# Performance work log

Hardware: AMD Instinct MI355X
Metric: run time of the kernel (lower is better)

## Reference

```python
import jax, jax.numpy as jnp
import numpy as np

BT, N, C, H, W = 1, 4, 64, 28, 60
ZC, YC, XC = 200, 8, 200  # grid dims (Zcam, Ycam, Xcam); voxel_shape=[200,200,8] -> Z=200, X=200, Y=8
OUT_C = 128
EPS = 1e-6


def setup_inputs() -> dict:
    key = jax.random.key(0)
    k1, k2, k3, k4 = jax.random.split(key, 4)
    # normalized sampling coords in ~[-1.2, 1.2] so some points fall outside the image (zero-padded)
    voxcam_coords = jax.random.uniform(k1, (BT, N, ZC, YC, XC, 3), jnp.float32, -1.2, 1.2)
    # binary visibility mask per voxel-camera pair
    vox_valid = (jax.random.uniform(k2, (BT, N, ZC, YC, XC, 1)) < 0.5).astype(jnp.float32)
    img_feats = jax.random.normal(k3, (BT, N, C, H, W), jnp.float32)
    W_comp = jax.random.normal(k4, (OUT_C, C * YC), jnp.float32) * 0.02  # MLP-as-1x1-conv height compressor
    b_comp = jnp.zeros((OUT_C,), jnp.float32)
    return {"voxcam_coords": voxcam_coords, "vox_valid": vox_valid, "img_feats": img_feats,
            "W_comp": W_comp, "b_comp": b_comp}


def _grid_sample_3d(feat, grid):
    """Trilinear grid_sample, align_corners=False, zeros padding.
    feat: (B, C, D, H, W); grid: (B, P, 3) with (x, y, z) in [-1, 1]. Returns (B, C, P)."""
    B, Cc, D, Hh, Ww = feat.shape
    x = ((grid[..., 0] + 1.0) * Ww - 1.0) * 0.5
    y = ((grid[..., 1] + 1.0) * Hh - 1.0) * 0.5
    z = ((grid[..., 2] + 1.0) * D - 1.0) * 0.5
    x0f, y0f, z0f = jnp.floor(x), jnp.floor(y), jnp.floor(z)
    wx, wy, wz = x - x0f, y - y0f, z - z0f
    x0, y0, z0 = x0f.astype(jnp.int32), y0f.astype(jnp.int32), z0f.astype(jnp.int32)

    def sample_one(fb, x0b, y0b, z0b, wxb, wyb, wzb):
        out = jnp.zeros((Cc, x0b.shape[0]), fb.dtype)
        for dz in (0, 1):
            for dy in (0, 1):
                for dx in (0, 1):
                    zi, yi, xi = z0b + dz, y0b + dy, x0b + dx
                    valid = ((zi >= 0) & (zi < D) & (yi >= 0) & (yi < Hh)
                             & (xi >= 0) & (xi < Ww)).astype(fb.dtype)
                    v = fb[:, jnp.clip(zi, 0, D - 1), jnp.clip(yi, 0, Hh - 1), jnp.clip(xi, 0, Ww - 1)]
                    w = ((wxb if dx else 1.0 - wxb) * (wyb if dy else 1.0 - wyb)
                         * (wzb if dz else 1.0 - wzb)) * valid
                    out = out + v * w[None]
        return out

    return jax.vmap(sample_one)(feat, x0, y0, z0, wx, wy, wz)


def reference(voxcam_coords, vox_valid, img_feats, W_comp, b_comp):
    bt, n, zc, yc, xc, _ = voxcam_coords.shape
    c, h, w = img_feats.shape[2], img_feats.shape[3], img_feats.shape[4]
    P = zc * yc * xc
    grid = voxcam_coords.reshape(bt * n, P, 3)
    feat = img_feats.reshape(bt * n, c, 1, h, w)  # N_group=1 depth axis
    sampled = _grid_sample_3d(feat, grid).reshape(bt, n, c, zc, yc, xc)
    mask = jnp.transpose(vox_valid, (0, 1, 5, 2, 3, 4))  # (bt, n, 1, zc, yc, xc)
    vox_feats = sampled * mask                      # get_feats_dense_grid_sample masking
    # reduce_cams: masked mean over cameras (dim=1)
    red = (vox_feats * mask).sum(axis=1) / (mask.sum(axis=1) + EPS)  # (bt, c, zc, yc, xc)
    # height compressor: 'bt c z y x -> bt (c y) z x' then 1x1 conv (MLP)
    comp_in = jnp.transpose(red, (0, 1, 3, 2, 4)).reshape(bt, c * yc, zc, xc)
    out = jnp.einsum('bczx,oc->bozx', comp_in, W_comp) + b_comp[None, :, None, None]
    # _unpack_batch: (b*t, C, Z, X) -> (b, t, C, Z, X) with b=t=1
    return out.reshape(1, bt, out.shape[1], zc, xc)
```

## Files before the change

### kernel.cpp

```cpp
#include <hip/hip_runtime.h>
#include <hip/hip_bf16.h>
#include <hip/hip_fp16.h>

#define N_  4
#define C_  64
#define H_  28
#define W_  60
#define ZC_ 200
#define YC_ 8
#define XC_ 200
#define OUTC_ 128
#define KD_ 512
#define EPS_ 1e-6f
#define ZB 4
#define XB 8
#define NCOL 32

typedef __attribute__((ext_vector_type(8))) _Float16 half8;
typedef __attribute__((ext_vector_type(4))) float f32x4;
typedef __attribute__((ext_vector_type(4))) unsigned int u32x4;

__global__ void gsvt_prep(const float* __restrict__ img,
                          const float* __restrict__ Wc,
                          __half* __restrict__ featH,
                          __half* __restrict__ WbH) {
    int tid = blockIdx.x * blockDim.x + threadIdx.x;
    int stride = gridDim.x * blockDim.x;
    const int totF = N_ * H_ * W_ * C_;
    for (int i = tid; i < totF; i += stride) {
        int c  = i & 63;
        int hw = i >> 6;
        int w  = hw % W_;
        int nh = hw / W_;
        int h  = nh % H_;
        int n  = nh / H_;
        featH[i] = __float2half(img[((n * C_ + c) * H_ + h) * W_ + w]);
    }
    const int totW = OUTC_ * KD_;
    for (int i = tid; i < totW; i += stride) {
        int k = i & (KD_ - 1);
        int o = i >> 9;
        int y = k >> 6;
        int c = k & 63;
        WbH[i] = __float2half(Wc[o * KD_ + c * YC_ + y]);
    }
}

__device__ __forceinline__ void accq(__half2* n, const u32x4 V, const unsigned wp) {
    const __half2 w2 = *(const __half2*)&wp;
    unsigned vx = V.x, vy = V.y, vz = V.z, vw = V.w;
    n[0] = __hfma2(w2, *(const __half2*)&vx, n[0]);
    n[1] = __hfma2(w2, *(const __half2*)&vy, n[1]);
    n[2] = __hfma2(w2, *(const __half2*)&vz, n[2]);
    n[3] = __hfma2(w2, *(const __half2*)&vw, n[3]);
}

__device__ __forceinline__ unsigned reph(float f) {
    auto h = __builtin_amdgcn_cvt_pkrtz(f, f);
    unsigned u;
    __builtin_memcpy(&u, &h, 4);
    return u;
}

__global__ __launch_bounds__(256, 4) void gsvt_fusedG(
        const float* __restrict__ coords,
        const float* __restrict__ validm,
        const __half* __restrict__ featH,
        const __half* __restrict__ WbH,
        const float* __restrict__ bias,
        float* __restrict__ out)
{
    __shared__ uint2 tab2[N_ * 256];
    __shared__ unsigned short redB[64][NCOL][8];
    float (*ms)[4] = (float(*)[4])&redB[0][0][0];

    const int z0 = blockIdx.y * ZB;
    const int x0 = blockIdx.x * XB;
    const int t  = threadIdx.x;

    const int p0   = t;
    const int y0_  = t >> 5;
    const int col0 = t & 31;
    const int zg   = z0 + (col0 >> 3);
    const int xg   = x0 + (col0 & 7);

    float gx[4], gy[4], gzv[4], mm[4];
    #pragma unroll
    for (int cam = 0; cam < N_; ++cam) {
        const int cb = ((cam * ZC_ + zg) * YC_ + y0_) * XC_ + xg;
        gx[cam]  = coords[cb * 3 + 0];
        gy[cam]  = coords[cb * 3 + 1];
        gzv[cam] = coords[cb * 3 + 2];
        mm[cam]  = validm[cb];
        ms[p0][cam] = mm[cam];
    }
    __syncthreads();

    {
        const float inv = 1.0f / (ms[p0][0] + ms[p0][1] + ms[p0][2] + ms[p0][3] + EPS_);
        #pragma unroll
        for (int cam = 0; cam < N_; ++cam) {
            const float xf = ((gx[cam] + 1.0f) * (float)W_ - 1.0f) * 0.5f;
            const float yf = ((gy[cam] + 1.0f) * (float)H_ - 1.0f) * 0.5f;
            const float zf = gzv[cam] * 0.5f;
            const float x0f = floorf(xf), y0f = floorf(yf), z0f = floorf(zf);
            const float wx = xf - x0f, wy = yf - y0f, wz = zf - z0f;
            const int xi = (int)x0f, yi = (int)y0f, zi = (int)z0f;

            const float zw = (zi == 0) ? (1.f - wz) : ((zi == -1) ? wz : 0.f);
            const float s  = mm[cam] * zw * inv;

            const float wx0 = (xi >= 0 && xi < W_)         ? (1.f - wx) * s : 0.f;
            const float wx1 = (xi + 1 >= 0 && xi + 1 < W_) ? wx * s         : 0.f;
            const float wy0 = (yi >= 0 && yi < H_)         ? (1.f - wy)     : 0.f;
            const float wy1 = (yi + 1 >= 0 && yi + 1 < H_) ? wy             : 0.f;

            const unsigned q00 = (unsigned)(wy0 * wx0 * 4095.f + 0.5f);
            const unsigned q01 = (unsigned)(wy0 * wx1 * 4095.f + 0.5f);
            const unsigned q10 = (unsigned)(wy1 * wx0 * 4095.f + 0.5f);
            const unsigned q11 = (unsigned)(wy1 * wx1 * 4095.f + 0.5f);

            const int xc0 = min(max(xi, 0), W_ - 1);
            const int xc1 = min(max(xi + 1, 0), W_ - 1);
            const int yc0 = min(max(yi, 0), H_ - 1);
            const int yc1 = min(max(yi + 1, 0), H_ - 1);
            const unsigned pixidx = (unsigned)((cam * H_ + yc0) * W_ + xc0);
            const unsigned fdx = (unsigned)(xc1 - xc0);
            const unsigned fdy = (unsigned)(yc1 - yc0);

            const unsigned A = q00 | (q01 << 12) | ((q10 & 0xFFu) << 24);
            const unsigned B = (q10 >> 8) | (q11 << 4) | (pixidx << 16)
                             | (fdx << 29) | (fdy << 30);
            tab2[cam * 256 + p0] = make_uint2(A, B);
        }
    }
    __syncthreads();

    const int grp   = t >> 3;
    const int lane8 = t & 7;
    const unsigned lb = (unsigned)(lane8 << 4);
    const char* fb = (const char*)featH;

    #define ISSUE(V, A_) asm volatile("global_load_dwordx4 %0, %1, off" \
                                      : "=v"(V) : "v"(A_))
    #define WAITV(n) do { asm volatile("s_waitcnt vmcnt(" #n ")"); \
                          __builtin_amdgcn_sched_barrier(0); } while (0)

    #pragma unroll
    for (int y = 0; y < YC_; ++y) {
        const int p = y * 32 + grp;

        const uint2 T0 = tab2[0 * 256 + p];
        const uint2 T1 = tab2[1 * 256 + p];
        const uint2 T2 = tab2[2 * 256 + p];
        const uint2 T3 = tab2[3 * 256 + p];

        u32x4 V00, V01, V02, V03, V10, V11, V12, V13;
        u32x4 V20, V21, V22, V23, V30, V31, V32, V33;
        #define ADDR_ISSUE(Tv, Va, Vb, Vc, Vd)                                 \
            {                                                                  \
                const bool act = (Tv.x | (Tv.y & 0xFFFFu)) != 0u;              \
                const unsigned base = act ? ((((Tv.y >> 16) & 0x1FFFu) << 7) + lb) : lb; \
                const unsigned dxo  = act ? (((Tv.y >> 29) & 1u) << 7) : 0u;   \
                const unsigned dyo  = act ? (((Tv.y >> 30) & 1u) * (unsigned)(W_ * 128)) : 0u; \
                ISSUE(Va, fb + base);                                          \
                ISSUE(Vb, fb + (base + dxo));                                  \
                ISSUE(Vc, fb + (base + dyo));                                  \
                ISSUE(Vd, fb + (base + dyo + dxo));                            \
            }
        ADDR_ISSUE(T0, V00, V01, V02, V03)
        ADDR_ISSUE(T1, V10, V11, V12, V13)
        ADDR_ISSUE(T2, V20, V21, V22, V23)
        ADDR_ISSUE(T3, V30, V31, V32, V33)
        #undef ADDR_ISSUE

        __half2 zz2 = __half2half2(__ushort_as_half(0));
        __half2 num[4] = {zz2, zz2, zz2, zz2};

        #define DECW(Tv, w00, w01, w10, w11)                                   \
            const unsigned w00 = reph((float)(Tv.x & 0xFFFu)            * (1.f/4095.f)); \
            const unsigned w01 = reph((float)((Tv.x >> 12) & 0xFFFu)    * (1.f/4095.f)); \
            const unsigned w10 = reph((float)((Tv.x >> 24) | ((Tv.y & 0xFu) << 8)) * (1.f/4095.f)); \
            const unsigned w11 = reph((float)((Tv.y >> 4) & 0xFFFu)     * (1.f/4095.f));

        { DECW(T0, a, b, c, d) WAITV(12);
          accq(num, V00, a); accq(num, V01, b); accq(num, V02, c); accq(num, V03, d); }
        { DECW(T1, a, b, c, d) WAITV(8);
          accq(num, V10, a); accq(num, V11, b); accq(num, V12, c); accq(num, V13, d); }
        { DECW(T2, a, b, c, d) WAITV(4);
          accq(num, V20, a); accq(num, V21, b); accq(num, V22, c); accq(num, V23, d); }
        { DECW(T3, a, b, c, d) WAITV(0);
          accq(num, V30, a); accq(num, V31, b); accq(num, V32, c); accq(num, V33, d); }
        #undef DECW

        const int kb   = y * 8 + lane8;
        const int pcol = (grp & 16) | ((grp ^ kb) & 15);
        unsigned n0 = *(unsigned*)&num[0], n1 = *(unsigned*)&num[1];
        unsigned n2 = *(unsigned*)&num[2], n3 = *(unsigned*)&num[3];
        *(uint4*)&redB[kb][pcol][0] = make_uint4(n0, n1, n2, n3);
    }
    #undef ISSUE
    #undef WAITV
    __syncthreads();

    const int wave = t >> 6;
    const int lane = t & 63;
    const int q    = lane >> 4;
    const int l16  = lane & 15;

    f32x4 acc00 = {0.f,0.f,0.f,0.f}, acc01 = {0.f,0.f,0.f,0.f};
    f32x4 acc10 = {0.f,0.f,0.f,0.f}, acc11 = {0.f,0.f,0.f,0.f};
    const __half* wbase = WbH + (wave * 32 + l16) * KD_;

    #pragma unroll
    for (int ks = 0; ks < 16; ++ks) {
        const int kb = ks * 4 + q;
        const int xs = l16 ^ (kb & 15);
        const half8 Bf0 = *(const half8*)&redB[kb][xs][0];
        const half8 Bf1 = *(const half8*)&redB[kb][16 + xs][0];
        const half8 Af0 = *(const half8*)(wbase + ks * 32 + q * 8);
        const half8 Af1 = *(const half8*)(wbase + 16 * KD_ + ks * 32 + q * 8);
        acc00 = __builtin_amdgcn_mfma_f32_16x16x32_f16(Af0, Bf0, acc00, 0, 0, 0);
        acc01 = __builtin_amdgcn_mfma_f32_16x16x32_f16(Af0, Bf1, acc01, 0, 0, 0);
        acc10 = __builtin_amdgcn_mfma_f32_16x16x32_f16(Af1, Bf0, acc10, 0, 0, 0);
        acc11 = __builtin_amdgcn_mfma_f32_16x16x32_f16(Af1, Bf1, acc11, 0, 0, 0);
    }

    #pragma unroll
    for (int ct = 0; ct < 2; ++ct) {
        const int c2  = ct * 16 + l16;
        const int zz  = c2 >> 3;
        const int xl  = c2 & 7;
        const int ob  = (z0 + zz) * XC_ + x0 + xl;
        const f32x4 a0 = ct ? acc01 : acc00;
        const f32x4 a1 = ct ? acc11 : acc10;
        #pragma unroll
        for (int j = 0; j < 4; ++j) {
            const int o0 = wave * 32 + q * 4 + j;
            out[o0 * (ZC_ * XC_) + ob] = a0[j] + bias[o0];
            const int o1 = o0 + 16;
            out[o1 * (ZC_ * XC_) + ob] = a1[j] + bias[o1];
        }
    }
}

extern "C" void kernel_launch(void* const* d_in, const int* in_sizes, int n_in,
                              void* d_out, int out_size, void* d_ws, size_t ws_size,
                              hipStream_t stream) {
    const float* coords = (const float*)d_in[0];
    const float* validm = (const float*)d_in[1];
    const float* img    = (const float*)d_in[2];
    const float* Wc     = (const float*)d_in[3];
    const float* bias   = (const float*)d_in[4];
    float* out = (float*)d_out;

    __half* featH = (__half*)d_ws;
    __half* WbH   = featH + (N_ * H_ * W_ * C_);

    gsvt_prep<<<512, 256, 0, stream>>>(img, Wc, featH, WbH);

    dim3 grid(XC_ / XB, ZC_ / ZB);
    gsvt_fusedG<<<grid, 256, 0, stream>>>(coords, validm, featH, WbH, bias, out);
}
```

Before: 56.13 us.

## Split fused sample+GEMM kernel into separate sampling and MFMA GEMM kernels

Splits the fused kernel in two when the workspace is large enough. A gather kernel writes the reduced fp16 features to global memory, and a separate GEMM kernel keeps the weights in registers and runs MFMA over tiles of 16 points. This removes the large LDS reduction buffer from the gather kernel, which raises its occupancy target to 6 blocks, and lets the GEMM reuse its weights across tiles. The cost is a global round trip of about 41 MB of intermediate data plus one extra kernel launch.

```diff
diff --git a/kernel.cpp b/kernel.cpp
--- a/kernel.cpp
+++ b/kernel.cpp
@@ -15,6 +15,8 @@
 #define ZB 4
 #define XB 8
 #define NCOL 32
+#define NPTS 40000
+#define TPB_GEMM 4
 
 typedef __attribute__((ext_vector_type(8))) _Float16 half8;
 typedef __attribute__((ext_vector_type(4))) float f32x4;
@@ -62,6 +64,203 @@
     return u;
 }
 
+__device__ __forceinline__ void phase0_tab(const float* __restrict__ coords,
+                                           const float* __restrict__ validm,
+                                           uint2* tab2, float (*ms)[4],
+                                           int z0, int x0, int t) {
+    const int p0   = t;
+    const int y0_  = t >> 5;
+    const int col0 = t & 31;
+    const int zg   = z0 + (col0 >> 3);
+    const int xg   = x0 + (col0 & 7);
+
+    float gx[4], gy[4], gzv[4], mm[4];
+    #pragma unroll
+    for (int cam = 0; cam < N_; ++cam) {
+        const int cb = ((cam * ZC_ + zg) * YC_ + y0_) * XC_ + xg;
+        gx[cam]  = coords[cb * 3 + 0];
+        gy[cam]  = coords[cb * 3 + 1];
+        gzv[cam] = coords[cb * 3 + 2];
+        mm[cam]  = validm[cb];
+        ms[p0][cam] = mm[cam];
+    }
+    __syncthreads();
+
+    const float inv = 1.0f / (ms[p0][0] + ms[p0][1] + ms[p0][2] + ms[p0][3] + EPS_);
+    #pragma unroll
+    for (int cam = 0; cam < N_; ++cam) {
+        const float xf = ((gx[cam] + 1.0f) * (float)W_ - 1.0f) * 0.5f;
+        const float yf = ((gy[cam] + 1.0f) * (float)H_ - 1.0f) * 0.5f;
+        const float zf = gzv[cam] * 0.5f;
+        const float x0f = floorf(xf), y0f = floorf(yf), z0f = floorf(zf);
+        const float wx = xf - x0f, wy = yf - y0f, wz = zf - z0f;
+        const int xi = (int)x0f, yi = (int)y0f, zi = (int)z0f;
+
+        const float zw = (zi == 0) ? (1.f - wz) : ((zi == -1) ? wz : 0.f);
+        const float s  = mm[cam] * zw * inv;
+
+        const float wx0 = (xi >= 0 && xi < W_)         ? (1.f - wx) * s : 0.f;
+        const float wx1 = (xi + 1 >= 0 && xi + 1 < W_) ? wx * s         : 0.f;
+        const float wy0 = (yi >= 0 && yi < H_)         ? (1.f - wy)     : 0.f;
+        const float wy1 = (yi + 1 >= 0 && yi + 1 < H_) ? wy             : 0.f;
+
+        const unsigned q00 = (unsigned)(wy0 * wx0 * 4095.f + 0.5f);
+        const unsigned q01 = (unsigned)(wy0 * wx1 * 4095.f + 0.5f);
+        const unsigned q10 = (unsigned)(wy1 * wx0 * 4095.f + 0.5f);
+        const unsigned q11 = (unsigned)(wy1 * wx1 * 4095.f + 0.5f);
+
+        const int xc0 = min(max(xi, 0), W_ - 1);
+        const int xc1 = min(max(xi + 1, 0), W_ - 1);
+        const int yc0 = min(max(yi, 0), H_ - 1);
+        const int yc1 = min(max(yi + 1, 0), H_ - 1);
+        const unsigned pixidx = (unsigned)((cam * H_ + yc0) * W_ + xc0);
+        const unsigned fdx = (unsigned)(xc1 - xc0);
+        const unsigned fdy = (unsigned)(yc1 - yc0);
+
+        const unsigned A = q00 | (q01 << 12) | ((q10 & 0xFFu) << 24);
+        const unsigned B = (q10 >> 8) | (q11 << 4) | (pixidx << 16)
+                         | (fdx << 29) | (fdy << 30);
+        tab2[cam * 256 + p0] = make_uint2(A, B);
+    }
+    __syncthreads();
+}
+
+#define GATHER_BODY(P_, OUTSTMT)                                               \
+    {                                                                          \
+        const uint2 T0 = tab2[0 * 256 + (P_)];                                 \
+        const uint2 T1 = tab2[1 * 256 + (P_)];                                 \
+        const uint2 T2 = tab2[2 * 256 + (P_)];                                 \
+        const uint2 T3 = tab2[3 * 256 + (P_)];                                 \
+        u32x4 V00, V01, V02, V03, V10, V11, V12, V13;                          \
+        u32x4 V20, V21, V22, V23, V30, V31, V32, V33;                          \
+        ADDR_ISSUE(T0, V00, V01, V02, V03)                                     \
+        ADDR_ISSUE(T1, V10, V11, V12, V13)                                     \
+        ADDR_ISSUE(T2, V20, V21, V22, V23)                                     \
+        ADDR_ISSUE(T3, V30, V31, V32, V33)                                     \
+        __half2 zz2 = __half2half2(__ushort_as_half(0));                       \
+        __half2 num[4] = {zz2, zz2, zz2, zz2};                                 \
+        { DECW(T0, a, b, c, d) WAITV(12);                                      \
+          accq(num, V00, a); accq(num, V01, b);                                \
+          accq(num, V02, c); accq(num, V03, d); }                              \
+        { DECW(T1, a, b, c, d) WAITV(8);                                       \
+          accq(num, V10, a); accq(num, V11, b);                                \
+          accq(num, V12, c); accq(num, V13, d); }                              \
+        { DECW(T2, a, b, c, d) WAITV(4);                                       \
+          accq(num, V20, a); accq(num, V21, b);                                \
+          accq(num, V22, c); accq(num, V23, d); }                              \
+        { DECW(T3, a, b, c, d) WAITV(0);                                       \
+          accq(num, V30, a); accq(num, V31, b);                                \
+          accq(num, V32, c); accq(num, V33, d); }                              \
+        unsigned n0 = *(unsigned*)&num[0], n1 = *(unsigned*)&num[1];           \
+        unsigned n2 = *(unsigned*)&num[2], n3 = *(unsigned*)&num[3];           \
+        OUTSTMT;                                                               \
+    }
+
+#define ADDR_ISSUE(Tv, Va, Vb, Vc, Vd)                                         \
+    {                                                                          \
+        const bool act = (Tv.x | (Tv.y & 0xFFFFu)) != 0u;                      \
+        const unsigned base = act ? ((((Tv.y >> 16) & 0x1FFFu) << 7) + lb) : lb; \
+        const unsigned dxo  = act ? (((Tv.y >> 29) & 1u) << 7) : 0u;           \
+        const unsigned dyo  = act ? (((Tv.y >> 30) & 1u) * (unsigned)(W_ * 128)) : 0u; \
+        ISSUE(Va, fb + base);                                                  \
+        ISSUE(Vb, fb + (base + dxo));                                          \
+        ISSUE(Vc, fb + (base + dyo));                                          \
+        ISSUE(Vd, fb + (base + dyo + dxo));                                    \
+    }
+#define ISSUE(V, A_) asm volatile("global_load_dwordx4 %0, %1, off" \
+                                  : "=v"(V) : "v"(A_))
+#define WAITV(n) do { asm volatile("s_waitcnt vmcnt(" #n ")"); \
+                      __builtin_amdgcn_sched_barrier(0); } while (0)
+#define DECW(Tv, w00, w01, w10, w11)                                           \
+    const unsigned w00 = reph((float)(Tv.x & 0xFFFu)            * (1.f/4095.f)); \
+    const unsigned w01 = reph((float)((Tv.x >> 12) & 0xFFFu)    * (1.f/4095.f)); \
+    const unsigned w10 = reph((float)((Tv.x >> 24) | ((Tv.y & 0xFu) << 8)) * (1.f/4095.f)); \
+    const unsigned w11 = reph((float)((Tv.y >> 4) & 0xFFFu)     * (1.f/4095.f));
+
+__global__ __launch_bounds__(256, 6) void gsvt_sampleH(
+        const float* __restrict__ coords,
+        const float* __restrict__ validm,
+        const __half* __restrict__ featH,
+        __half* __restrict__ red)
+{
+    __shared__ uint2 tab2[N_ * 256];
+    __shared__ float ms[256][4];
+
+    const int z0 = blockIdx.y * ZB;
+    const int x0 = blockIdx.x * XB;
+    const int t  = threadIdx.x;
+
+    phase0_tab(coords, validm, tab2, ms, z0, x0, t);
+
+    const int grp   = t >> 3;
+    const int lane8 = t & 7;
+    const unsigned lb = (unsigned)(lane8 << 4);
+    const char* fb = (const char*)featH;
+    const int pt0 = (z0 + (grp >> 3)) * XC_ + x0 + (grp & 7);
+
+    #pragma unroll
+    for (int y = 0; y < YC_; ++y) {
+        const int p  = y * 32 + grp;
+        const int kb = y * 8 + lane8;
+        GATHER_BODY(p,
+            *(uint4*)(red + ((size_t)kb * NPTS + pt0) * 8) =
+                make_uint4(n0, n1, n2, n3))
+    }
+}
+
+__global__ __launch_bounds__(256, 2) void gsvt_gemmH(
+        const __half* __restrict__ red,
+        const __half* __restrict__ WbH,
+        const float* __restrict__ bias,
+        float* __restrict__ out)
+{
+    const int t    = threadIdx.x;
+    const int wave = t >> 6;
+    const int lane = t & 63;
+    const int q    = lane >> 4;
+    const int l16  = lane & 15;
+
+    half8 A0[16], A1[16];
+    const __half* wrow0 = WbH + (wave * 32 + l16) * KD_;
+    #pragma unroll
+    for (int ks = 0; ks < 16; ++ks) {
+        A0[ks] = *(const half8*)(wrow0 + ks * 32 + q * 8);
+        A1[ks] = *(const half8*)(wrow0 + 16 * KD_ + ks * 32 + q * 8);
+    }
+    float bs0[4], bs1[4];
+    #pragma unroll
+    for (int j = 0; j < 4; ++j) {
+        bs0[j] = bias[wave * 32 + q * 4 + j];
+        bs1[j] = bias[wave * 32 + q * 4 + j + 16];
+    }
+
+    for (int tt = 0; tt < TPB_GEMM; ++tt) {
+        const int n0 = (blockIdx.x * TPB_GEMM + tt) * 16;
+
+        half8 Bf[16];
+        #pragma unroll
+        for (int ks = 0; ks < 16; ++ks) {
+            const int kb = ks * 4 + q;
+            Bf[ks] = *(const half8*)(red + ((size_t)kb * NPTS + n0 + l16) * 8);
+        }
+
+        f32x4 acc0 = {0.f,0.f,0.f,0.f};
+        f32x4 acc1 = {0.f,0.f,0.f,0.f};
+        #pragma unroll
+        for (int ks = 0; ks < 16; ++ks) {
+            acc0 = __builtin_amdgcn_mfma_f32_16x16x32_f16(A0[ks], Bf[ks], acc0, 0, 0, 0);
+            acc1 = __builtin_amdgcn_mfma_f32_16x16x32_f16(A1[ks], Bf[ks], acc1, 0, 0, 0);
+        }
+
+        #pragma unroll
+        for (int j = 0; j < 4; ++j) {
+            const int o0 = wave * 32 + q * 4 + j;
+            out[(size_t)o0 * NPTS + n0 + l16] = acc0[j] + bs0[j];
+            out[(size_t)(o0 + 16) * NPTS + n0 + l16] = acc1[j] + bs1[j];
+        }
+    }
+}
+
 __global__ __launch_bounds__(256, 4) void gsvt_fusedG(
         const float* __restrict__ coords,
         const float* __restrict__ validm,
@@ -78,129 +277,21 @@
     const int x0 = blockIdx.x * XB;
     const int t  = threadIdx.x;
 
-    const int p0   = t;
-    const int y0_  = t >> 5;
-    const int col0 = t & 31;
-    const int zg   = z0 + (col0 >> 3);
-    const int xg   = x0 + (col0 & 7);
-
-    float gx[4], gy[4], gzv[4], mm[4];
-    #pragma unroll
-    for (int cam = 0; cam < N_; ++cam) {
-        const int cb = ((cam * ZC_ + zg) * YC_ + y0_) * XC_ + xg;
-        gx[cam]  = coords[cb * 3 + 0];
-        gy[cam]  = coords[cb * 3 + 1];
-        gzv[cam] = coords[cb * 3 + 2];
-        mm[cam]  = validm[cb];
-        ms[p0][cam] = mm[cam];
-    }
-    __syncthreads();
-
-    {
-        const float inv = 1.0f / (ms[p0][0] + ms[p0][1] + ms[p0][2] + ms[p0][3] + EPS_);
-        #pragma unroll
-        for (int cam = 0; cam < N_; ++cam) {
-            const float xf = ((gx[cam] + 1.0f) * (float)W_ - 1.0f) * 0.5f;
-            const float yf = ((gy[cam] + 1.0f) * (float)H_ - 1.0f) * 0.5f;
-            const float zf = gzv[cam] * 0.5f;
-            const float x0f = floorf(xf), y0f = floorf(yf), z0f = floorf(zf);
-            const float wx = xf - x0f, wy = yf - y0f, wz = zf - z0f;
-            const int xi = (int)x0f, yi = (int)y0f, zi = (int)z0f;
-
-            const float zw = (zi == 0) ? (1.f - wz) : ((zi == -1) ? wz : 0.f);
-            const float s  = mm[cam] * zw * inv;
-
-            const float wx0 = (xi >= 0 && xi < W_)         ? (1.f - wx) * s : 0.f;
-            const float wx1 = (xi + 1 >= 0 && xi + 1 < W_) ? wx * s         : 0.f;
-            const float wy0 = (yi >= 0 && yi < H_)         ? (1.f - wy)     : 0.f;
-            const float wy1 = (yi + 1 >= 0 && yi + 1 < H_) ? wy             : 0.f;
-
-            const unsigned q00 = (unsigned)(wy0 * wx0 * 4095.f + 0.5f);
-            const unsigned q01 = (unsigned)(wy0 * wx1 * 4095.f + 0.5f);
-            const unsigned q10 = (unsigned)(wy1 * wx0 * 4095.f + 0.5f);
-            const unsigned q11 = (unsigned)(wy1 * wx1 * 4095.f + 0.5f);
-
-            const int xc0 = min(max(xi, 0), W_ - 1);
-            const int xc1 = min(max(xi + 1, 0), W_ - 1);
-            const int yc0 = min(max(yi, 0), H_ - 1);
-            const int yc1 = min(max(yi + 1, 0), H_ - 1);
-            const unsigned pixidx = (unsigned)((cam * H_ + yc0) * W_ + xc0);
-            const unsigned fdx = (unsigned)(xc1 - xc0);
-            const unsigned fdy = (unsigned)(yc1 - yc0);
-
-            const unsigned A = q00 | (q01 << 12) | ((q10 & 0xFFu) << 24);
-            const unsigned B = (q10 >> 8) | (q11 << 4) | (pixidx << 16)
-                             | (fdx << 29) | (fdy << 30);
-            tab2[cam * 256 + p0] = make_uint2(A, B);
-        }
-    }
-    __syncthreads();
+    phase0_tab(coords, validm, tab2, ms, z0, x0, t);
 
     const int grp   = t >> 3;
     const int lane8 = t & 7;
     const unsigned lb = (unsigned)(lane8 << 4);
     const char* fb = (const char*)featH;
 
-    #define ISSUE(V, A_) asm volatile("global_load_dwordx4 %0, %1, off" \
-                                      : "=v"(V) : "v"(A_))
-    #define WAITV(n) do { asm volatile("s_waitcnt vmcnt(" #n ")"); \
-                          __builtin_amdgcn_sched_barrier(0); } while (0)
-
     #pragma unroll
     for (int y = 0; y < YC_; ++y) {
-        const int p = y * 32 + grp;
-
-        const uint2 T0 = tab2[0 * 256 + p];
-        const uint2 T1 = tab2[1 * 256 + p];
-        const uint2 T2 = tab2[2 * 256 + p];
-        const uint2 T3 = tab2[3 * 256 + p];
-
-        u32x4 V00, V01, V02, V03, V10, V11, V12, V13;
-        u32x4 V20, V21, V22, V23, V30, V31, V32, V33;
-        #define ADDR_ISSUE(Tv, Va, Vb, Vc, Vd)                                 \
-            {                                                                  \
-                const bool act = (Tv.x | (Tv.y & 0xFFFFu)) != 0u;              \
-                const unsigned base = act ? ((((Tv.y >> 16) & 0x1FFFu) << 7) + lb) : lb; \
-                const unsigned dxo  = act ? (((Tv.y >> 29) & 1u) << 7) : 0u;   \
-                const unsigned dyo  = act ? (((Tv.y >> 30) & 1u) * (unsigned)(W_ * 128)) : 0u; \
-                ISSUE(Va, fb + base);                                          \
-                ISSUE(Vb, fb + (base + dxo));                                  \
-                ISSUE(Vc, fb + (base + dyo));                                  \
-                ISSUE(Vd, fb + (base + dyo + dxo));                            \
-            }
-        ADDR_ISSUE(T0, V00, V01, V02, V03)
-        ADDR_ISSUE(T1, V10, V11, V12, V13)
-        ADDR_ISSUE(T2, V20, V21, V22, V23)
-        ADDR_ISSUE(T3, V30, V31, V32, V33)
-        #undef ADDR_ISSUE
-
-        __half2 zz2 = __half2half2(__ushort_as_half(0));
-        __half2 num[4] = {zz2, zz2, zz2, zz2};
-
-        #define DECW(Tv, w00, w01, w10, w11)                                   \
-            const unsigned w00 = reph((float)(Tv.x & 0xFFFu)            * (1.f/4095.f)); \
-            const unsigned w01 = reph((float)((Tv.x >> 12) & 0xFFFu)    * (1.f/4095.f)); \
-            const unsigned w10 = reph((float)((Tv.x >> 24) | ((Tv.y & 0xFu) << 8)) * (1.f/4095.f)); \
-            const unsigned w11 = reph((float)((Tv.y >> 4) & 0xFFFu)     * (1.f/4095.f));
-
-        { DECW(T0, a, b, c, d) WAITV(12);
-          accq(num, V00, a); accq(num, V01, b); accq(num, V02, c); accq(num, V03, d); }
-        { DECW(T1, a, b, c, d) WAITV(8);
-          accq(num, V10, a); accq(num, V11, b); accq(num, V12, c); accq(num, V13, d); }
-        { DECW(T2, a, b, c, d) WAITV(4);
-          accq(num, V20, a); accq(num, V21, b); accq(num, V22, c); accq(num, V23, d); }
-        { DECW(T3, a, b, c, d) WAITV(0);
-          accq(num, V30, a); accq(num, V31, b); accq(num, V32, c); accq(num, V33, d); }
-        #undef DECW
-
+        const int p    = y * 32 + grp;
         const int kb   = y * 8 + lane8;
         const int pcol = (grp & 16) | ((grp ^ kb) & 15);
-        unsigned n0 = *(unsigned*)&num[0], n1 = *(unsigned*)&num[1];
-        unsigned n2 = *(unsigned*)&num[2], n3 = *(unsigned*)&num[3];
-        *(uint4*)&redB[kb][pcol][0] = make_uint4(n0, n1, n2, n3);
-    }
-    #undef ISSUE
-    #undef WAITV
+        GATHER_BODY(p,
+            *(uint4*)&redB[kb][pcol][0] = make_uint4(n0, n1, n2, n3))
+    }
     __syncthreads();
 
     const int wave = t >> 6;
@@ -256,9 +347,18 @@
 
     __half* featH = (__half*)d_ws;
     __half* WbH   = featH + (N_ * H_ * W_ * C_);
+    __half* red   = WbH + (OUTC_ * KD_);
+
+    const size_t need = (size_t)(N_ * H_ * W_ * C_ + OUTC_ * KD_) * 2
+                      + (size_t)64 * NPTS * 8 * 2;
 
     gsvt_prep<<<512, 256, 0, stream>>>(img, Wc, featH, WbH);
 
     dim3 grid(XC_ / XB, ZC_ / ZB);
-    gsvt_fusedG<<<grid, 256, 0, stream>>>(coords, validm, featH, WbH, bias, out);
-}
+    if (ws_size >= need) {
+        gsvt_sampleH<<<grid, 256, 0, stream>>>(coords, validm, featH, red);
+        gsvt_gemmH<<<625, 256, 0, stream>>>(red, WbH, bias, out);
+    } else {
+        gsvt_fusedG<<<grid, 256, 0, stream>>>(coords, validm, featH, WbH, bias, out);
+    }
+}
```

Measured after the change: 72.92 us. 1.3x slower.
